# Kernel tuning notes

Hardware: AMD Instinct MI355X
Metric: run time of the kernel (lower is better)

Reference implementation:

```python
import jax, jax.numpy as jnp
import numpy as np

B, N, DIM = 4, 1024, 1024
H, D = 16, 64          # num_heads, head_dim
SW = 256               # sliding_window
ROPE_BASE = 10000.0
LN_EPS = 1e-5


def _layernorm(x, w, b):
    mu = jnp.mean(x, axis=-1, keepdims=True)
    var = jnp.mean((x - mu) ** 2, axis=-1, keepdims=True)
    return (x - mu) * jax.lax.rsqrt(var + LN_EPS) * w + b


def _rotate_half(x):
    x1, x2 = jnp.split(x, 2, axis=-1)
    return jnp.concatenate([-x2, x1], axis=-1)


def setup_inputs() -> dict:
    key = jax.random.key(0)
    ks = jax.random.split(key, 8)
    s = 0.02
    return {
        "x": jax.random.normal(ks[0], (B, N, DIM), dtype=jnp.float32),
        "qkv_w": jax.random.normal(ks[1], (3 * H * D, DIM), dtype=jnp.float32) * s,
        "qn_w": jnp.ones((D,), jnp.float32),
        "qn_b": jnp.zeros((D,), jnp.float32),
        "kn_w": jnp.ones((D,), jnp.float32),
        "kn_b": jnp.zeros((D,), jnp.float32),
        "sinks": jax.random.normal(ks[2], (H,), dtype=jnp.float32),
        "proj_w": jax.random.normal(ks[3], (DIM, H * D), dtype=jnp.float32) * s,
        "proj_b": jnp.zeros((DIM,), jnp.float32),
    }


def reference(x, qkv_w, qn_w, qn_b, kn_w, kn_b, sinks, proj_w, proj_b):
    Bx, Nx, _ = x.shape
    # fused QKV projection -> [3, B, H, N, D]
    qkv = (x @ qkv_w.T).reshape(Bx, Nx, 3, H, D).transpose(2, 0, 3, 1, 4)
    q, k, v = qkv[0], qkv[1], qkv[2]
    # qk-norm (LayerNorm over head_dim)
    q = _layernorm(q, qn_w, qn_b)
    k = _layernorm(k, kn_w, kn_b)
    # 1d RoPE (DeepseekV3-style: emb = cat(freqs, freqs), rotate_half)
    inv_freq = 1.0 / (ROPE_BASE ** (jnp.arange(0, D, 2, dtype=jnp.float32) / D))
    freqs = jnp.arange(Nx, dtype=jnp.float32)[:, None] * inv_freq[None, :]  # [N, D/2]
    emb = jnp.concatenate([freqs, freqs], axis=-1)                           # [N, D]
    cos, sin = jnp.cos(emb), jnp.sin(emb)
    q = q * cos + _rotate_half(q) * sin
    k = k * cos + _rotate_half(k) * sin
    # sliding-window causal mask with attention sinks
    sm_scale = 1.0 / np.sqrt(D)
    scores = jnp.einsum("bhqd,bhkd->bhqk", q, k) * sm_scale  # [B,H,N,N]
    i = jnp.arange(Nx)[:, None]
    j = jnp.arange(Nx)[None, :]
    allowed = (j <= i) & (j > i - SW)
    scores = jnp.where(allowed, scores, -jnp.inf)
    # append sink logit per head, softmax, drop sink column
    sink_col = jnp.broadcast_to(sinks[None, :, None, None], (Bx, H, Nx, 1))
    logits = jnp.concatenate([scores, sink_col], axis=-1)
    probs = jax.nn.softmax(logits, axis=-1)[..., :-1]
    out = jnp.einsum("bhqk,bhkd->bhqd", probs, v)
    out = out.transpose(0, 2, 1, 3).reshape(Bx, Nx, H * D)
    return out @ proj_w.T + proj_b
```

## Files before the change

### kernel.cpp

```cpp
#include <hip/hip_runtime.h>
#include <stdint.h>

typedef unsigned short u16;
typedef __bf16 bf16x8 __attribute__((ext_vector_type(8)));
typedef float f32x4 __attribute__((ext_vector_type(4)));

__device__ __forceinline__ float b2f(u16 u) {
  union { uint32_t i; float f; } x; x.i = ((uint32_t)u) << 16; return x.f;
}
__device__ __forceinline__ u16 f2b(float f) {
  union { float f; uint32_t i; } x; x.f = f;
  uint32_t r = x.i + 0x7fffu + ((x.i >> 16) & 1u);
  return (u16)(r >> 16);
}
__device__ __forceinline__ void gload_lds16(const u16* g, u16* l) {
  __builtin_amdgcn_global_load_lds(
      (const __attribute__((address_space(1))) void*)g,
      (__attribute__((address_space(3))) void*)l, 16, 0, 0);
}

__launch_bounds__(256)
__global__ void cvt_bf16(const float* __restrict__ x, const float* __restrict__ wq,
                         const float* __restrict__ wp, u16* __restrict__ dst) {
  const int i = (blockIdx.x * 256 + threadIdx.x) * 4;
  const float* src; int off;
  if (i < 4194304)      { src = x;  off = i; }
  else if (i < 7340032) { src = wq; off = i - 4194304; }
  else                  { src = wp; off = i - 7340032; }
  const float4 v = *(const float4*)(src + off);
  ushort4 o;
  o.x = f2b(v.x); o.y = f2b(v.y); o.z = f2b(v.z); o.w = f2b(v.w);
  *(ushort4*)(dst + i) = o;
}

__launch_bounds__(256)
__global__ void rope_tab(float* __restrict__ tab) {
  const int tid = blockIdx.x * 256 + threadIdx.x;
  const int pos = tid >> 6, d = tid & 63, i = d & 31;
  const float f = pos * exp2f(i * -0.41524101186092029f);
  float s, c;
  sincosf(f, &s, &c);
  *(float2*)(tab + tid * 2) = make_float2(c, s);
}

template<int MODE>
__launch_bounds__(256)
__global__ void gemm128(const u16* __restrict__ A, const u16* __restrict__ Bw,
                        void* __restrict__ Cp, const float* __restrict__ bias, int K) {
  __shared__ __align__(16) u16 As[128 * 32];
  __shared__ __align__(16) u16 Bs[128 * 32];
  const int t = threadIdx.x;
  const int w = t >> 6, l = t & 63, lr = l & 15, lg = l >> 4;
  const int m0 = blockIdx.y * 128, n0 = blockIdx.x * 128;
  const int wm = (w >> 1) * 64, wn = (w & 1) * 64;
  const int srow = w * 32 + (l >> 2);
  const int scol = (l & 3) * 8;
  const u16* ga0 = A  + (m0 + srow) * K + scol;
  const u16* ga1 = ga0 + 16 * K;
  const u16* gb0 = Bw + (n0 + srow) * K + scol;
  const u16* gb1 = gb0 + 16 * K;
  u16* la0 = As + w * 1024;
  u16* la1 = As + w * 1024 + 512;
  u16* lb0 = Bs + w * 1024;
  u16* lb1 = Bs + w * 1024 + 512;

  f32x4 acc[4][4] = {};
  const int nk = K >> 5;
  for (int kt = 0; kt < nk; ++kt) {
    const int ko = kt * 32;
    __syncthreads();
    gload_lds16(ga0 + ko, la0);
    gload_lds16(ga1 + ko, la1);
    gload_lds16(gb0 + ko, lb0);
    gload_lds16(gb1 + ko, lb1);
    __syncthreads();
    bf16x8 af[4], bfr[4];
#pragma unroll
    for (int i = 0; i < 4; ++i)
      af[i] = *(const bf16x8*)(As + (wm + i * 16 + lr) * 32 + lg * 8);
#pragma unroll
    for (int j = 0; j < 4; ++j)
      bfr[j] = *(const bf16x8*)(Bs + (wn + j * 16 + lr) * 32 + lg * 8);
#pragma unroll
    for (int i = 0; i < 4; ++i)
#pragma unroll
      for (int j = 0; j < 4; ++j)
        acc[i][j] = __builtin_amdgcn_mfma_f32_16x16x32_bf16(af[i], bfr[j], acc[i][j], 0, 0, 0);
  }
#pragma unroll
  for (int i = 0; i < 4; ++i)
#pragma unroll
    for (int j = 0; j < 4; ++j)
#pragma unroll
      for (int r = 0; r < 4; ++r) {
        const int gm = m0 + wm + i * 16 + lg * 4 + r;
        const int gn = n0 + wn + j * 16 + lr;
        const float v = acc[i][j][r];
        if (MODE == 0) {
          const int which = gn >> 10, hh = (gn >> 6) & 15, dd = gn & 63;
          const int bb = gm >> 10, pp = gm & 1023;
          ((u16*)Cp)[which * 4194304 + ((bb * 16 + hh) << 16) + (pp << 6) + dd] = f2b(v);
        } else {
          ((float*)Cp)[(gm << 10) + gn] = v + bias[gn];
        }
      }
}

__launch_bounds__(256)
__global__ void ln_rope(u16* __restrict__ qk, const float* __restrict__ qn_w,
                        const float* __restrict__ qn_b, const float* __restrict__ kn_w,
                        const float* __restrict__ kn_b, const float* __restrict__ tab) {
  const int t = threadIdx.x, l = t & 63;
  const int wv = blockIdx.x * 4 + (t >> 6);
  const int row = wv * 8 + (l >> 3);
  const int c = l & 7;
  const int which = row >> 16;
  const int pos = row & 1023;
  const float* wgt = which ? kn_w : qn_w;
  const float* bia = which ? kn_b : qn_b;
  const u16* src = qk + row * 64 + c * 8;
  const ushort4 ra = *(const ushort4*)(src);
  const ushort4 rb = *(const ushort4*)(src + 4);
  float v[8] = {b2f(ra.x), b2f(ra.y), b2f(ra.z), b2f(ra.w),
                b2f(rb.x), b2f(rb.y), b2f(rb.z), b2f(rb.w)};
  float s = 0.f;
#pragma unroll
  for (int i = 0; i < 8; ++i) s += v[i];
#pragma unroll
  for (int off = 1; off < 8; off <<= 1) s += __shfl_xor(s, off);
  const float mu = s * 0.015625f;
  float e[8], qs = 0.f;
#pragma unroll
  for (int i = 0; i < 8; ++i) { e[i] = v[i] - mu; qs += e[i] * e[i]; }
#pragma unroll
  for (int off = 1; off < 8; off <<= 1) qs += __shfl_xor(qs, off);
  const float rstd = rsqrtf(qs * 0.015625f + 1e-5f);
  const int d0 = c * 8;
  float wb[8], bb[8];
  *(float4*)(wb) = *(const float4*)(wgt + d0);
  *(float4*)(wb + 4) = *(const float4*)(wgt + d0 + 4);
  *(float4*)(bb) = *(const float4*)(bia + d0);
  *(float4*)(bb + 4) = *(const float4*)(bia + d0 + 4);
  float n[8], r[8];
#pragma unroll
  for (int i = 0; i < 8; ++i) n[i] = e[i] * rstd * wb[i] + bb[i];
#pragma unroll
  for (int i = 0; i < 8; ++i) r[i] = __shfl_xor(n[i], 4);
  const bool lo = (c < 4);
#pragma unroll
  for (int i = 0; i < 8; ++i) r[i] = lo ? -r[i] : r[i];
  float cs[16];
  *(float4*)(cs)      = *(const float4*)(tab + (pos * 64 + d0) * 2);
  *(float4*)(cs + 4)  = *(const float4*)(tab + (pos * 64 + d0) * 2 + 4);
  *(float4*)(cs + 8)  = *(const float4*)(tab + (pos * 64 + d0) * 2 + 8);
  *(float4*)(cs + 12) = *(const float4*)(tab + (pos * 64 + d0) * 2 + 12);
  ushort4 oa, ob;
  float o[8];
#pragma unroll
  for (int i = 0; i < 8; ++i) o[i] = n[i] * cs[2 * i] + r[i] * cs[2 * i + 1];
  oa.x = f2b(o[0]); oa.y = f2b(o[1]); oa.z = f2b(o[2]); oa.w = f2b(o[3]);
  ob.x = f2b(o[4]); ob.y = f2b(o[5]); ob.z = f2b(o[6]); ob.w = f2b(o[7]);
  const int dstc = which ? (c ^ (pos & 7)) : c;
  u16* dst = qk + row * 64 + dstc * 8;
  *(ushort4*)(dst) = oa;
  *(ushort4*)(dst + 4) = ob;
}

__launch_bounds__(256)
__global__ void vtrans(const u16* __restrict__ v, u16* __restrict__ vt) {
  __shared__ u16 tile[128 * 65];
  const int t = threadIdx.x;
  const int bh = blockIdx.x >> 3;
  const int n0 = (blockIdx.x & 7) * 128;
  const u16* src = v + bh * 65536 + n0 * 64;
#pragma unroll
  for (int it = 0; it < 8; ++it) {
    const int e = (it * 256 + t) * 4;
    const int n = e >> 6, d = e & 63;
    const ushort4 x = *(const ushort4*)(src + n * 64 + d);
    tile[n * 65 + d + 0] = x.x;
    tile[n * 65 + d + 1] = x.y;
    tile[n * 65 + d + 2] = x.z;
    tile[n * 65 + d + 3] = x.w;
  }
  __syncthreads();
  u16* dst = vt + bh * 65536;
#pragma unroll
  for (int it = 0; it < 8; ++it) {
    const int o = (it * 256 + t) * 4;
    const int d = o >> 7, c = o & 127;
    ushort4 y;
    y.x = tile[(c + 0) * 65 + d];
    y.y = tile[(c + 1) * 65 + d];
    y.z = tile[(c + 2) * 65 + d];
    y.w = tile[(c + 3) * 65 + d];
    const int gj = n0 + c;
    const int nb = gj >> 6, jl = gj & 63;
    const int slot = (jl >> 3) ^ (d & 7);
    *(ushort4*)(dst + nb * 4096 + d * 64 + slot * 8 + (jl & 7)) = y;
  }
}

__launch_bounds__(256, 2)
__global__ void attn_kernel(const u16* __restrict__ q, const u16* __restrict__ k,
                            const u16* __restrict__ vt, const float* __restrict__ sinks,
                            u16* __restrict__ ao) {
  __shared__ __align__(16) u16 Ks[20480];
  __shared__ __align__(16) u16 Vs[20480];
  const int t = threadIdx.x, w = t >> 6, l = t & 63, lr = l & 15, lg = l >> 4;
  const int bid = blockIdx.x;
  const int qb = bid & 15, h = (bid >> 4) & 15, b = bid >> 8;
  const int i0 = qb * 64 + w * 16;
  const int bh = b * 16 + h;
  const u16* qp = q + bh * 65536;
  const u16* kp = k + bh * 65536;
  const u16* vp = vt + bh * 65536;
  const int j0 = qb * 64 - 256;

#pragma unroll
  for (int i = 0; i < 10; ++i) {
    const int c = w * 10 + i;
    int off = j0 * 64 + c * 512 + l * 8;
    off = off < 0 ? 0 : off;
    gload_lds16(kp + off, Ks + c * 512);
  }
#pragma unroll
  for (int i = 0; i < 10; ++i) {
    const int c = w * 10 + i;
    const int n = c >> 3, p = c & 7;
    int nb = qb - 4 + n;
    nb = nb < 0 ? 0 : nb;
    gload_lds16(vp + nb * 4096 + p * 512 + l * 8, Vs + c * 512);
  }
  const bf16x8 qf0 = *(const bf16x8*)(qp + (i0 + lr) * 64 + lg * 8);
  const bf16x8 qf1 = *(const bf16x8*)(qp + (i0 + lr) * 64 + 32 + lg * 8);
  __syncthreads();

  const int key = lr & 7;
  f32x4 sacc[17];
#pragma unroll
  for (int jt = 0; jt < 17; ++jt) {
    const int r = w * 16 + jt * 16 + lr;
    const bf16x8 kf0 = *(const bf16x8*)(Ks + r * 64 + ((lg ^ key)) * 8);
    const bf16x8 kf1 = *(const bf16x8*)(Ks + r * 64 + (((lg + 4) ^ key)) * 8);
    f32x4 a = {0.f, 0.f, 0.f, 0.f};
    a = __builtin_amdgcn_mfma_f32_16x16x32_bf16(qf0, kf0, a, 0, 0, 0);
    a = __builtin_amdgcn_mfma_f32_16x16x32_bf16(qf1, kf1, a, 0, 0, 0);
    sacc[jt] = a;
  }
  const float sink = sinks[h];
  const int ja = i0 - 256;
  float mx[4] = {-1e30f, -1e30f, -1e30f, -1e30f};
#pragma unroll
  for (int jt = 0; jt < 17; ++jt)
#pragma unroll
    for (int r = 0; r < 4; ++r) {
      const int qi = i0 + lg * 4 + r;
      const int jg = ja + jt * 16 + lr;
      const bool ok = (jg >= 0) && (jg <= qi) && (jg > qi - 256);
      const float sv = ok ? sacc[jt][r] * 0.125f : -1e30f;
      sacc[jt][r] = sv;
      mx[r] = fmaxf(mx[r], sv);
    }
#pragma unroll
  for (int off = 1; off < 16; off <<= 1)
#pragma unroll
    for (int r = 0; r < 4; ++r) mx[r] = fmaxf(mx[r], __shfl_xor(mx[r], off));
#pragma unroll
  for (int r = 0; r < 4; ++r) mx[r] = fmaxf(mx[r], sink);
  float sum[4] = {0.f, 0.f, 0.f, 0.f};
#pragma unroll
  for (int jt = 0; jt < 17; ++jt)
#pragma unroll
    for (int r = 0; r < 4; ++r) {
      const float e = __expf(sacc[jt][r] - mx[r]);
      sacc[jt][r] = e;
      sum[r] += e;
    }
#pragma unroll
  for (int off = 1; off < 16; off <<= 1)
#pragma unroll
    for (int r = 0; r < 4; ++r) sum[r] += __shfl_xor(sum[r], off);
  float inv[4];
#pragma unroll
  for (int r = 0; r < 4; ++r) inv[r] = 1.0f / (sum[r] + __expf(sink - mx[r]));

  __syncthreads();
  u16* pb = Ks + w * 4736;
  {
    ushort4 z; z.x = 0; z.y = 0; z.z = 0; z.w = 0;
    *(ushort4*)(pb + (l >> 2) * 296 + 272 + (l & 3) * 4) = z;
  }
#pragma unroll
  for (int jt = 0; jt < 17; ++jt)
#pragma unroll
    for (int r = 0; r < 4; ++r)
      pb[(lg * 4 + r) * 296 + jt * 16 + lr] = f2b(sacc[jt][r] * inv[r]);

  f32x4 oacc[4] = {};
#pragma unroll
  for (int ks = 0; ks < 9; ++ks) {
    const bf16x8 pf = *(const bf16x8*)(pb + lr * 296 + ks * 32 + lg * 8);
#pragma unroll
    for (int dt = 0; dt < 4; ++dt) {
      int r = w * 16 + ks * 32 + lg * 8;
      r = r < 320 ? r : 0;
      const int n = r >> 6, jl = r & 63;
      const int slot = (jl >> 3) ^ (lr & 7);
      const bf16x8 vf = *(const bf16x8*)(Vs + n * 4096 + (dt * 16 + lr) * 64 + slot * 8);
      oacc[dt] = __builtin_amdgcn_mfma_f32_16x16x32_bf16(pf, vf, oacc[dt], 0, 0, 0);
    }
  }
#pragma unroll
  for (int dt = 0; dt < 4; ++dt)
#pragma unroll
    for (int r = 0; r < 4; ++r) {
      const int m = (b << 10) + i0 + lg * 4 + r;
      ao[(m << 10) + (h << 6) + dt * 16 + lr] = f2b(oacc[dt][r]);
    }
}

extern "C" void kernel_launch(void* const* d_in, const int* in_sizes, int n_in,
                              void* d_out, int out_size, void* d_ws, size_t ws_size,
                              hipStream_t stream) {
  const float* x      = (const float*)d_in[0];
  const float* qkv_w  = (const float*)d_in[1];
  const float* qn_w   = (const float*)d_in[2];
  const float* qn_b   = (const float*)d_in[3];
  const float* kn_w   = (const float*)d_in[4];
  const float* kn_b   = (const float*)d_in[5];
  const float* sinks  = (const float*)d_in[6];
  const float* proj_w = (const float*)d_in[7];
  const float* proj_b = (const float*)d_in[8];
  float* out = (float*)d_out;
  u16* ws     = (u16*)d_ws;
  u16* qkv    = ws;
  u16* xb     = ws + 12582912;
  u16* wqkvb  = ws + 16777216;
  u16* wprojb = ws + 19922944;
  float* tab  = (float*)(ws + 20971520);
  u16* ao     = ws + 21233664;
  u16* vtw    = ws + 12582912;

  cvt_bf16<<<8192, 256, 0, stream>>>(x, qkv_w, proj_w, xb);
  rope_tab<<<256, 256, 0, stream>>>(tab);
  gemm128<0><<<dim3(24, 32), 256, 0, stream>>>(xb, wqkvb, qkv, nullptr, 1024);
  ln_rope<<<4096, 256, 0, stream>>>(qkv, qn_w, qn_b, kn_w, kn_b, tab);
  vtrans<<<512, 256, 0, stream>>>(qkv + 8388608, vtw);
  attn_kernel<<<1024, 256, 0, stream>>>(qkv, qkv + 4194304, vtw, sinks, ao);
  gemm128<1><<<dim3(8, 32), 256, 0, stream>>>(ao, wprojb, out, proj_b, 1024);
}
```

Measured before the change: 199.3 us.

## Fuse qk-LayerNorm and RoPE into QKV GEMM epilogue, widen K tile, swizzle LDS

The fp32-to-bf16 conversion and the RoPE table build are merged into one prep kernel. That kernel also writes the bf16 operands in an XOR-swizzled 8-element-slot layout. The QKV GEMM now loads 64-wide K tiles and reads LDS with the matching swizzle to avoid bank conflicts, and it applies LayerNorm and RoPE for q/k in its epilogue through intra-row shuffles. This removes the separate ln_rope pass over q and k. The attention output is also written swizzled so the projection GEMM can read it the same way, at the cost of more complex address math and a larger LDS footprint.

Result: no change. 199.7 us (+0.2%).

```diff
diff --git a/kernel.cpp b/kernel.cpp
--- a/kernel.cpp
+++ b/kernel.cpp
@@ -13,6 +13,14 @@
   uint32_t r = x.i + 0x7fffu + ((x.i >> 16) & 1u);
   return (u16)(r >> 16);
 }
+__device__ __forceinline__ uint4 pk8(const float4 a, const float4 b) {
+  uint4 r;
+  r.x = (uint32_t)f2b(a.x) | ((uint32_t)f2b(a.y) << 16);
+  r.y = (uint32_t)f2b(a.z) | ((uint32_t)f2b(a.w) << 16);
+  r.z = (uint32_t)f2b(b.x) | ((uint32_t)f2b(b.y) << 16);
+  r.w = (uint32_t)f2b(b.z) | ((uint32_t)f2b(b.w) << 16);
+  return r;
+}
 __device__ __forceinline__ void gload_lds16(const u16* g, u16* l) {
   __builtin_amdgcn_global_load_lds(
       (const __attribute__((address_space(1))) void*)g,
@@ -20,150 +28,159 @@
 }
 
 __launch_bounds__(256)
-__global__ void cvt_bf16(const float* __restrict__ x, const float* __restrict__ wq,
-                         const float* __restrict__ wp, u16* __restrict__ dst) {
-  const int i = (blockIdx.x * 256 + threadIdx.x) * 4;
-  const float* src; int off;
-  if (i < 4194304)      { src = x;  off = i; }
-  else if (i < 7340032) { src = wq; off = i - 4194304; }
-  else                  { src = wp; off = i - 7340032; }
-  const float4 v = *(const float4*)(src + off);
-  ushort4 o;
-  o.x = f2b(v.x); o.y = f2b(v.y); o.z = f2b(v.z); o.w = f2b(v.w);
-  *(ushort4*)(dst + i) = o;
-}
-
-__launch_bounds__(256)
-__global__ void rope_tab(float* __restrict__ tab) {
-  const int tid = blockIdx.x * 256 + threadIdx.x;
-  const int pos = tid >> 6, d = tid & 63, i = d & 31;
-  const float f = pos * exp2f(i * -0.41524101186092029f);
-  float s, c;
-  sincosf(f, &s, &c);
-  *(float2*)(tab + tid * 2) = make_float2(c, s);
+__global__ void prep(const float* __restrict__ x, const float* __restrict__ wq,
+                     const float* __restrict__ wp, u16* __restrict__ dst,
+                     float* __restrict__ tab) {
+  if (blockIdx.x >= 4096) {
+    const int tid = (blockIdx.x - 4096) * 256 + threadIdx.x;
+    const int pos = tid >> 5, idx = tid & 31;
+    const float f = pos * exp2f(idx * -0.41524101186092029f);
+    float s, c;
+    sincosf(f, &s, &c);
+    *(float2*)(tab + tid * 2) = make_float2(c, s);
+    return;
+  }
+  const int i = (blockIdx.x * 256 + threadIdx.x) * 8;
+  const float* src; int local, base;
+  if (i < 4194304)      { src = x;  local = i;           base = 0; }
+  else if (i < 7340032) { src = wq; local = i - 4194304; base = 4194304; }
+  else                  { src = wp; local = i - 7340032; base = 7340032; }
+  const int row = local >> 10, col = local & 1023;
+  const int slot = ((col >> 3) & 7) ^ (row & 7);
+  const float4 a = *(const float4*)(src + local);
+  const float4 b = *(const float4*)(src + local + 4);
+  *(uint4*)(dst + base + row * 1024 + (col & ~63) + slot * 8) = pk8(a, b);
 }
 
 template<int MODE>
 __launch_bounds__(256)
 __global__ void gemm128(const u16* __restrict__ A, const u16* __restrict__ Bw,
-                        void* __restrict__ Cp, const float* __restrict__ bias, int K) {
-  __shared__ __align__(16) u16 As[128 * 32];
-  __shared__ __align__(16) u16 Bs[128 * 32];
+                        void* __restrict__ Cp, const float* __restrict__ bias,
+                        const float* __restrict__ qn_w, const float* __restrict__ qn_b,
+                        const float* __restrict__ kn_w, const float* __restrict__ kn_b,
+                        const float* __restrict__ tab, int K) {
+  __shared__ __align__(16) u16 As[128 * 64];
+  __shared__ __align__(16) u16 Bs[128 * 64];
   const int t = threadIdx.x;
   const int w = t >> 6, l = t & 63, lr = l & 15, lg = l >> 4;
   const int m0 = blockIdx.y * 128, n0 = blockIdx.x * 128;
   const int wm = (w >> 1) * 64, wn = (w & 1) * 64;
-  const int srow = w * 32 + (l >> 2);
-  const int scol = (l & 3) * 8;
-  const u16* ga0 = A  + (m0 + srow) * K + scol;
-  const u16* ga1 = ga0 + 16 * K;
-  const u16* gb0 = Bw + (n0 + srow) * K + scol;
-  const u16* gb1 = gb0 + 16 * K;
-  u16* la0 = As + w * 1024;
-  u16* la1 = As + w * 1024 + 512;
-  u16* lb0 = Bs + w * 1024;
-  u16* lb1 = Bs + w * 1024 + 512;
+  const int srow = w * 32 + (l >> 3);
+  const int scol = (l & 7) * 8;
+  const u16* gA = A  + (m0 + srow) * K + scol;
+  const u16* gB = Bw + (n0 + srow) * K + scol;
 
   f32x4 acc[4][4] = {};
-  const int nk = K >> 5;
+  const int nk = K >> 6;
   for (int kt = 0; kt < nk; ++kt) {
-    const int ko = kt * 32;
+    const int ko = kt * 64;
     __syncthreads();
-    gload_lds16(ga0 + ko, la0);
-    gload_lds16(ga1 + ko, la1);
-    gload_lds16(gb0 + ko, lb0);
-    gload_lds16(gb1 + ko, lb1);
+#pragma unroll
+    for (int i = 0; i < 4; ++i)
+      gload_lds16(gA + i * 8 * K + ko, As + (w * 32 + i * 8) * 64);
+#pragma unroll
+    for (int i = 0; i < 4; ++i)
+      gload_lds16(gB + i * 8 * K + ko, Bs + (w * 32 + i * 8) * 64);
     __syncthreads();
-    bf16x8 af[4], bfr[4];
-#pragma unroll
-    for (int i = 0; i < 4; ++i)
-      af[i] = *(const bf16x8*)(As + (wm + i * 16 + lr) * 32 + lg * 8);
-#pragma unroll
-    for (int j = 0; j < 4; ++j)
-      bfr[j] = *(const bf16x8*)(Bs + (wn + j * 16 + lr) * 32 + lg * 8);
+    bf16x8 af0[4], af1[4], bf0[4], bf1[4];
+#pragma unroll
+    for (int i = 0; i < 4; ++i) {
+      const int ra = wm + i * 16 + lr;
+      const int sa = (lg ^ (ra & 7)) * 8;
+      af0[i] = *(const bf16x8*)(As + ra * 64 + sa);
+      af1[i] = *(const bf16x8*)(As + ra * 64 + (sa ^ 32));
+    }
+#pragma unroll
+    for (int j = 0; j < 4; ++j) {
+      const int rb = wn + j * 16 + lr;
+      const int sb = (lg ^ (rb & 7)) * 8;
+      bf0[j] = *(const bf16x8*)(Bs + rb * 64 + sb);
+      bf1[j] = *(const bf16x8*)(Bs + rb * 64 + (sb ^ 32));
+    }
+#pragma unroll
+    for (int i = 0; i < 4; ++i)
+#pragma unroll
+      for (int j = 0; j < 4; ++j) {
+        acc[i][j] = __builtin_amdgcn_mfma_f32_16x16x32_bf16(af0[i], bf0[j], acc[i][j], 0, 0, 0);
+        acc[i][j] = __builtin_amdgcn_mfma_f32_16x16x32_bf16(af1[i], bf1[j], acc[i][j], 0, 0, 0);
+      }
+  }
+
+  if (MODE == 1) {
 #pragma unroll
     for (int i = 0; i < 4; ++i)
 #pragma unroll
       for (int j = 0; j < 4; ++j)
-        acc[i][j] = __builtin_amdgcn_mfma_f32_16x16x32_bf16(af[i], bfr[j], acc[i][j], 0, 0, 0);
-  }
+#pragma unroll
+        for (int r = 0; r < 4; ++r) {
+          const int gm = m0 + wm + i * 16 + lg * 4 + r;
+          const int gn = n0 + wn + j * 16 + lr;
+          ((float*)Cp)[(gm << 10) + gn] = acc[i][j][r] + bias[gn];
+        }
+    return;
+  }
+  const int whichB = blockIdx.x >> 3;
+  const int hh = ((n0 + wn) >> 6) & 15;
+  u16* Cb = (u16*)Cp + whichB * 4194304;
+  if (whichB == 2) {
+#pragma unroll
+    for (int i = 0; i < 4; ++i)
+#pragma unroll
+      for (int j = 0; j < 4; ++j)
+#pragma unroll
+        for (int r = 0; r < 4; ++r) {
+          const int gm = m0 + wm + i * 16 + lg * 4 + r;
+          Cb[(((gm >> 10) * 16 + hh) << 16) + ((gm & 1023) << 6) + j * 16 + lr] =
+              f2b(acc[i][j][r]);
+        }
+    return;
+  }
+  const float* wl = whichB ? kn_w : qn_w;
+  const float* bl = whichB ? kn_b : qn_b;
+  float wln[4], bln[4];
+#pragma unroll
+  for (int j = 0; j < 4; ++j) { wln[j] = wl[j * 16 + lr]; bln[j] = bl[j * 16 + lr]; }
 #pragma unroll
   for (int i = 0; i < 4; ++i)
 #pragma unroll
-    for (int j = 0; j < 4; ++j)
-#pragma unroll
-      for (int r = 0; r < 4; ++r) {
-        const int gm = m0 + wm + i * 16 + lg * 4 + r;
-        const int gn = n0 + wn + j * 16 + lr;
-        const float v = acc[i][j][r];
-        if (MODE == 0) {
-          const int which = gn >> 10, hh = (gn >> 6) & 15, dd = gn & 63;
-          const int bb = gm >> 10, pp = gm & 1023;
-          ((u16*)Cp)[which * 4194304 + ((bb * 16 + hh) << 16) + (pp << 6) + dd] = f2b(v);
-        } else {
-          ((float*)Cp)[(gm << 10) + gn] = v + bias[gn];
+    for (int r = 0; r < 4; ++r) {
+      const int gm = m0 + wm + i * 16 + lg * 4 + r;
+      const int pos = gm & 1023;
+      float v0 = acc[i][0][r], v1 = acc[i][1][r], v2 = acc[i][2][r], v3 = acc[i][3][r];
+      float s = v0 + v1 + v2 + v3;
+#pragma unroll
+      for (int m = 1; m < 16; m <<= 1) s += __shfl_xor(s, m);
+      const float mu = s * 0.015625f;
+      const float d0 = v0 - mu, d1 = v1 - mu, d2 = v2 - mu, d3 = v3 - mu;
+      float qv = d0 * d0 + d1 * d1 + d2 * d2 + d3 * d3;
+#pragma unroll
+      for (int m = 1; m < 16; m <<= 1) qv += __shfl_xor(qv, m);
+      const float rstd = rsqrtf(qv * 0.015625f + 1e-5f);
+      float nn[4];
+      nn[0] = d0 * rstd * wln[0] + bln[0];
+      nn[1] = d1 * rstd * wln[1] + bln[1];
+      nn[2] = d2 * rstd * wln[2] + bln[2];
+      nn[3] = d3 * rstd * wln[3] + bln[3];
+      const float2 csA = *(const float2*)(tab + (pos * 32 + lr) * 2);
+      const float2 csB = *(const float2*)(tab + (pos * 32 + 16 + lr) * 2);
+      float o[4];
+      o[0] = nn[0] * csA.x - nn[2] * csA.y;
+      o[1] = nn[1] * csB.x - nn[3] * csB.y;
+      o[2] = nn[2] * csA.x + nn[0] * csA.y;
+      o[3] = nn[3] * csB.x + nn[1] * csB.y;
+      u16* cb = Cb + (((gm >> 10) * 16 + hh) << 16) + (pos << 6);
+      if (whichB == 1) {
+        const int key = pos & 7;
+#pragma unroll
+        for (int j = 0; j < 4; ++j) {
+          const int d = j * 16 + lr;
+          cb[((d >> 3) ^ key) * 8 + (d & 7)] = f2b(o[j]);
         }
+      } else {
+#pragma unroll
+        for (int j = 0; j < 4; ++j) cb[j * 16 + lr] = f2b(o[j]);
       }
-}
-
-__launch_bounds__(256)
-__global__ void ln_rope(u16* __restrict__ qk, const float* __restrict__ qn_w,
-                        const float* __restrict__ qn_b, const float* __restrict__ kn_w,
-                        const float* __restrict__ kn_b, const float* __restrict__ tab) {
-  const int t = threadIdx.x, l = t & 63;
-  const int wv = blockIdx.x * 4 + (t >> 6);
-  const int row = wv * 8 + (l >> 3);
-  const int c = l & 7;
-  const int which = row >> 16;
-  const int pos = row & 1023;
-  const float* wgt = which ? kn_w : qn_w;
-  const float* bia = which ? kn_b : qn_b;
-  const u16* src = qk + row * 64 + c * 8;
-  const ushort4 ra = *(const ushort4*)(src);
-  const ushort4 rb = *(const ushort4*)(src + 4);
-  float v[8] = {b2f(ra.x), b2f(ra.y), b2f(ra.z), b2f(ra.w),
-                b2f(rb.x), b2f(rb.y), b2f(rb.z), b2f(rb.w)};
-  float s = 0.f;
-#pragma unroll
-  for (int i = 0; i < 8; ++i) s += v[i];
-#pragma unroll
-  for (int off = 1; off < 8; off <<= 1) s += __shfl_xor(s, off);
-  const float mu = s * 0.015625f;
-  float e[8], qs = 0.f;
-#pragma unroll
-  for (int i = 0; i < 8; ++i) { e[i] = v[i] - mu; qs += e[i] * e[i]; }
-#pragma unroll
-  for (int off = 1; off < 8; off <<= 1) qs += __shfl_xor(qs, off);
-  const float rstd = rsqrtf(qs * 0.015625f + 1e-5f);
-  const int d0 = c * 8;
-  float wb[8], bb[8];
-  *(float4*)(wb) = *(const float4*)(wgt + d0);
-  *(float4*)(wb + 4) = *(const float4*)(wgt + d0 + 4);
-  *(float4*)(bb) = *(const float4*)(bia + d0);
-  *(float4*)(bb + 4) = *(const float4*)(bia + d0 + 4);
-  float n[8], r[8];
-#pragma unroll
-  for (int i = 0; i < 8; ++i) n[i] = e[i] * rstd * wb[i] + bb[i];
-#pragma unroll
-  for (int i = 0; i < 8; ++i) r[i] = __shfl_xor(n[i], 4);
-  const bool lo = (c < 4);
-#pragma unroll
-  for (int i = 0; i < 8; ++i) r[i] = lo ? -r[i] : r[i];
-  float cs[16];
-  *(float4*)(cs)      = *(const float4*)(tab + (pos * 64 + d0) * 2);
-  *(float4*)(cs + 4)  = *(const float4*)(tab + (pos * 64 + d0) * 2 + 4);
-  *(float4*)(cs + 8)  = *(const float4*)(tab + (pos * 64 + d0) * 2 + 8);
-  *(float4*)(cs + 12) = *(const float4*)(tab + (pos * 64 + d0) * 2 + 12);
-  ushort4 oa, ob;
-  float o[8];
-#pragma unroll
-  for (int i = 0; i < 8; ++i) o[i] = n[i] * cs[2 * i] + r[i] * cs[2 * i + 1];
-  oa.x = f2b(o[0]); oa.y = f2b(o[1]); oa.z = f2b(o[2]); oa.w = f2b(o[3]);
-  ob.x = f2b(o[4]); ob.y = f2b(o[5]); ob.z = f2b(o[6]); ob.w = f2b(o[7]);
-  const int dstc = which ? (c ^ (pos & 7)) : c;
-  u16* dst = qk + row * 64 + dstc * 8;
-  *(ushort4*)(dst) = oa;
-  *(ushort4*)(dst + 4) = ob;
+    }
 }
 
 __launch_bounds__(256)
@@ -316,7 +333,8 @@
 #pragma unroll
     for (int r = 0; r < 4; ++r) {
       const int m = (b << 10) + i0 + lg * 4 + r;
-      ao[(m << 10) + (h << 6) + dt * 16 + lr] = f2b(oacc[dt][r]);
+      const int cg = (dt * 2 + (lr >> 3)) ^ (m & 7);
+      ao[(m << 10) + (h << 6) + cg * 8 + (lr & 7)] = f2b(oacc[dt][r]);
     }
 }
 
@@ -336,17 +354,17 @@
   u16* ws     = (u16*)d_ws;
   u16* qkv    = ws;
   u16* xb     = ws + 12582912;
-  u16* wqkvb  = ws + 16777216;
   u16* wprojb = ws + 19922944;
   float* tab  = (float*)(ws + 20971520);
   u16* ao     = ws + 21233664;
   u16* vtw    = ws + 12582912;
 
-  cvt_bf16<<<8192, 256, 0, stream>>>(x, qkv_w, proj_w, xb);
-  rope_tab<<<256, 256, 0, stream>>>(tab);
-  gemm128<0><<<dim3(24, 32), 256, 0, stream>>>(xb, wqkvb, qkv, nullptr, 1024);
-  ln_rope<<<4096, 256, 0, stream>>>(qkv, qn_w, qn_b, kn_w, kn_b, tab);
+  prep<<<4224, 256, 0, stream>>>(x, qkv_w, proj_w, xb, tab);
+  gemm128<0><<<dim3(24, 32), 256, 0, stream>>>(xb, xb + 4194304, qkv, nullptr,
+                                               qn_w, qn_b, kn_w, kn_b, tab, 1024);
   vtrans<<<512, 256, 0, stream>>>(qkv + 8388608, vtw);
   attn_kernel<<<1024, 256, 0, stream>>>(qkv, qkv + 4194304, vtw, sinks, ao);
-  gemm128<1><<<dim3(8, 32), 256, 0, stream>>>(ao, wprojb, out, proj_b, 1024);
-}
+  gemm128<1><<<dim3(8, 32), 256, 0, stream>>>(ao, wprojb, out, proj_b,
+                                              nullptr, nullptr, nullptr, nullptr,
+                                              nullptr, 1024);
+}
```

## Fuse prep kernels, write V transposed from QKV GEMM, swizzle GEMM LDS layout

Applied to the files above, without the earlier changes.

Merges the bf16 conversion and RoPE table kernels into one launch, with the table halved to 32 entries per position. The QKV GEMM epilogue now writes V directly in the swizzled transposed layout, which removes the separate vtrans kernel and its round trip through memory. GEMM operands are pre-swizzled during conversion, and the attention output is written swizzled, so that LDS fragment reads avoid bank conflicts. The cost is scattered 2-byte stores in the V epilogue and a more complex write layout that every consumer must agree on.

After: 190.0 us. 1.05x faster.

```diff
diff --git a/kernel.cpp b/kernel.cpp
--- a/kernel.cpp
+++ b/kernel.cpp
@@ -13,6 +13,14 @@
   uint32_t r = x.i + 0x7fffu + ((x.i >> 16) & 1u);
   return (u16)(r >> 16);
 }
+__device__ __forceinline__ uint4 pk8(const float4 a, const float4 b) {
+  uint4 r;
+  r.x = (uint32_t)f2b(a.x) | ((uint32_t)f2b(a.y) << 16);
+  r.y = (uint32_t)f2b(a.z) | ((uint32_t)f2b(a.w) << 16);
+  r.z = (uint32_t)f2b(b.x) | ((uint32_t)f2b(b.y) << 16);
+  r.w = (uint32_t)f2b(b.z) | ((uint32_t)f2b(b.w) << 16);
+  return r;
+}
 __device__ __forceinline__ void gload_lds16(const u16* g, u16* l) {
   __builtin_amdgcn_global_load_lds(
       (const __attribute__((address_space(1))) void*)g,
@@ -20,33 +28,35 @@
 }
 
 __launch_bounds__(256)
-__global__ void cvt_bf16(const float* __restrict__ x, const float* __restrict__ wq,
-                         const float* __restrict__ wp, u16* __restrict__ dst) {
-  const int i = (blockIdx.x * 256 + threadIdx.x) * 4;
-  const float* src; int off;
-  if (i < 4194304)      { src = x;  off = i; }
-  else if (i < 7340032) { src = wq; off = i - 4194304; }
-  else                  { src = wp; off = i - 7340032; }
-  const float4 v = *(const float4*)(src + off);
-  ushort4 o;
-  o.x = f2b(v.x); o.y = f2b(v.y); o.z = f2b(v.z); o.w = f2b(v.w);
-  *(ushort4*)(dst + i) = o;
-}
-
-__launch_bounds__(256)
-__global__ void rope_tab(float* __restrict__ tab) {
-  const int tid = blockIdx.x * 256 + threadIdx.x;
-  const int pos = tid >> 6, d = tid & 63, i = d & 31;
-  const float f = pos * exp2f(i * -0.41524101186092029f);
-  float s, c;
-  sincosf(f, &s, &c);
-  *(float2*)(tab + tid * 2) = make_float2(c, s);
+__global__ void prep(const float* __restrict__ x, const float* __restrict__ wq,
+                     const float* __restrict__ wp, u16* __restrict__ dst,
+                     float* __restrict__ tab) {
+  if (blockIdx.x >= 4096) {
+    const int tid = (blockIdx.x - 4096) * 256 + threadIdx.x;
+    const int pos = tid >> 5, idx = tid & 31;
+    const float f = pos * exp2f(idx * -0.41524101186092029f);
+    float s, c;
+    sincosf(f, &s, &c);
+    *(float2*)(tab + tid * 2) = make_float2(c, s);
+    return;
+  }
+  const int i = (blockIdx.x * 256 + threadIdx.x) * 8;
+  const float* src; int local, base;
+  if (i < 4194304)      { src = x;  local = i;           base = 0; }
+  else if (i < 7340032) { src = wq; local = i - 4194304; base = 4194304; }
+  else                  { src = wp; local = i - 7340032; base = 7340032; }
+  const int row = local >> 10, col = local & 1023;
+  const int slot = ((col >> 3) & 3) ^ (row & 3);
+  const float4 a = *(const float4*)(src + local);
+  const float4 b = *(const float4*)(src + local + 4);
+  *(uint4*)(dst + base + (row << 10) + (col & ~31) + (slot << 3)) = pk8(a, b);
 }
 
 template<int MODE>
 __launch_bounds__(256)
 __global__ void gemm128(const u16* __restrict__ A, const u16* __restrict__ Bw,
-                        void* __restrict__ Cp, const float* __restrict__ bias, int K) {
+                        void* __restrict__ Cp, const float* __restrict__ bias,
+                        u16* __restrict__ vt, int K) {
   __shared__ __align__(16) u16 As[128 * 32];
   __shared__ __align__(16) u16 Bs[128 * 32];
   const int t = threadIdx.x;
@@ -76,17 +86,53 @@
     __syncthreads();
     bf16x8 af[4], bfr[4];
 #pragma unroll
-    for (int i = 0; i < 4; ++i)
-      af[i] = *(const bf16x8*)(As + (wm + i * 16 + lr) * 32 + lg * 8);
-#pragma unroll
-    for (int j = 0; j < 4; ++j)
-      bfr[j] = *(const bf16x8*)(Bs + (wn + j * 16 + lr) * 32 + lg * 8);
+    for (int i = 0; i < 4; ++i) {
+      const int ra = wm + i * 16 + lr;
+      af[i] = *(const bf16x8*)(As + ra * 32 + ((lg ^ (ra & 3)) << 3));
+    }
+#pragma unroll
+    for (int j = 0; j < 4; ++j) {
+      const int rb = wn + j * 16 + lr;
+      bfr[j] = *(const bf16x8*)(Bs + rb * 32 + ((lg ^ (rb & 3)) << 3));
+    }
 #pragma unroll
     for (int i = 0; i < 4; ++i)
 #pragma unroll
       for (int j = 0; j < 4; ++j)
         acc[i][j] = __builtin_amdgcn_mfma_f32_16x16x32_bf16(af[i], bfr[j], acc[i][j], 0, 0, 0);
   }
+  if (MODE == 1) {
+#pragma unroll
+    for (int i = 0; i < 4; ++i)
+#pragma unroll
+      for (int j = 0; j < 4; ++j)
+#pragma unroll
+        for (int r = 0; r < 4; ++r) {
+          const int gm = m0 + wm + i * 16 + lg * 4 + r;
+          const int gn = n0 + wn + j * 16 + lr;
+          ((float*)Cp)[(gm << 10) + gn] = acc[i][j][r] + bias[gn];
+        }
+    return;
+  }
+  const int whichB = blockIdx.x >> 3;
+  const int hh = ((n0 + wn) >> 6) & 15;
+  if (whichB == 2) {
+#pragma unroll
+    for (int i = 0; i < 4; ++i)
+#pragma unroll
+      for (int j = 0; j < 4; ++j)
+#pragma unroll
+        for (int r = 0; r < 4; ++r) {
+          const int gm = m0 + wm + i * 16 + lg * 4 + r;
+          const int bh = (gm >> 10) * 16 + hh;
+          const int pos = gm & 1023, nb = pos >> 6, jl = pos & 63;
+          const int d = j * 16 + lr;
+          vt[bh * 65536 + nb * 4096 + d * 64 + (((jl >> 3) ^ (d & 7)) << 3) + (jl & 7)] =
+              f2b(acc[i][j][r]);
+        }
+    return;
+  }
+  u16* Cb = (u16*)Cp + whichB * 4194304;
 #pragma unroll
   for (int i = 0; i < 4; ++i)
 #pragma unroll
@@ -94,15 +140,8 @@
 #pragma unroll
       for (int r = 0; r < 4; ++r) {
         const int gm = m0 + wm + i * 16 + lg * 4 + r;
-        const int gn = n0 + wn + j * 16 + lr;
-        const float v = acc[i][j][r];
-        if (MODE == 0) {
-          const int which = gn >> 10, hh = (gn >> 6) & 15, dd = gn & 63;
-          const int bb = gm >> 10, pp = gm & 1023;
-          ((u16*)Cp)[which * 4194304 + ((bb * 16 + hh) << 16) + (pp << 6) + dd] = f2b(v);
-        } else {
-          ((float*)Cp)[(gm << 10) + gn] = v + bias[gn];
-        }
+        Cb[(((gm >> 10) * 16 + hh) << 16) + ((gm & 1023) << 6) + j * 16 + lr] =
+            f2b(acc[i][j][r]);
       }
 }
 
@@ -150,10 +189,11 @@
 #pragma unroll
   for (int i = 0; i < 8; ++i) r[i] = lo ? -r[i] : r[i];
   float cs[16];
-  *(float4*)(cs)      = *(const float4*)(tab + (pos * 64 + d0) * 2);
-  *(float4*)(cs + 4)  = *(const float4*)(tab + (pos * 64 + d0) * 2 + 4);
-  *(float4*)(cs + 8)  = *(const float4*)(tab + (pos * 64 + d0) * 2 + 8);
-  *(float4*)(cs + 12) = *(const float4*)(tab + (pos * 64 + d0) * 2 + 12);
+  const int ti = (pos * 32 + (c & 3) * 8) * 2;
+  *(float4*)(cs)      = *(const float4*)(tab + ti);
+  *(float4*)(cs + 4)  = *(const float4*)(tab + ti + 4);
+  *(float4*)(cs + 8)  = *(const float4*)(tab + ti + 8);
+  *(float4*)(cs + 12) = *(const float4*)(tab + ti + 12);
   ushort4 oa, ob;
   float o[8];
 #pragma unroll
@@ -164,41 +204,6 @@
   u16* dst = qk + row * 64 + dstc * 8;
   *(ushort4*)(dst) = oa;
   *(ushort4*)(dst + 4) = ob;
-}
-
-__launch_bounds__(256)
-__global__ void vtrans(const u16* __restrict__ v, u16* __restrict__ vt) {
-  __shared__ u16 tile[128 * 65];
-  const int t = threadIdx.x;
-  const int bh = blockIdx.x >> 3;
-  const int n0 = (blockIdx.x & 7) * 128;
-  const u16* src = v + bh * 65536 + n0 * 64;
-#pragma unroll
-  for (int it = 0; it < 8; ++it) {
-    const int e = (it * 256 + t) * 4;
-    const int n = e >> 6, d = e & 63;
-    const ushort4 x = *(const ushort4*)(src + n * 64 + d);
-    tile[n * 65 + d + 0] = x.x;
-    tile[n * 65 + d + 1] = x.y;
-    tile[n * 65 + d + 2] = x.z;
-    tile[n * 65 + d + 3] = x.w;
-  }
-  __syncthreads();
-  u16* dst = vt + bh * 65536;
-#pragma unroll
-  for (int it = 0; it < 8; ++it) {
-    const int o = (it * 256 + t) * 4;
-    const int d = o >> 7, c = o & 127;
-    ushort4 y;
-    y.x = tile[(c + 0) * 65 + d];
-    y.y = tile[(c + 1) * 65 + d];
-    y.z = tile[(c + 2) * 65 + d];
-    y.w = tile[(c + 3) * 65 + d];
-    const int gj = n0 + c;
-    const int nb = gj >> 6, jl = gj & 63;
-    const int slot = (jl >> 3) ^ (d & 7);
-    *(ushort4*)(dst + nb * 4096 + d * 64 + slot * 8 + (jl & 7)) = y;
-  }
 }
 
 __launch_bounds__(256, 2)
@@ -316,7 +321,9 @@
 #pragma unroll
     for (int r = 0; r < 4; ++r) {
       const int m = (b << 10) + i0 + lg * 4 + r;
-      ao[(m << 10) + (h << 6) + dt * 16 + lr] = f2b(oacc[dt][r]);
+      const int d = dt * 16 + lr;
+      const int cg = ((d >> 3) & 3) ^ (m & 3);
+      ao[(m << 10) + (h << 6) + (d & ~31) + (cg << 3) + (d & 7)] = f2b(oacc[dt][r]);
     }
 }
 
@@ -335,18 +342,15 @@
   float* out = (float*)d_out;
   u16* ws     = (u16*)d_ws;
   u16* qkv    = ws;
+  u16* vtw    = ws + 8388608;
   u16* xb     = ws + 12582912;
-  u16* wqkvb  = ws + 16777216;
   u16* wprojb = ws + 19922944;
   float* tab  = (float*)(ws + 20971520);
   u16* ao     = ws + 21233664;
-  u16* vtw    = ws + 12582912;
-
-  cvt_bf16<<<8192, 256, 0, stream>>>(x, qkv_w, proj_w, xb);
-  rope_tab<<<256, 256, 0, stream>>>(tab);
-  gemm128<0><<<dim3(24, 32), 256, 0, stream>>>(xb, wqkvb, qkv, nullptr, 1024);
+
+  prep<<<4224, 256, 0, stream>>>(x, qkv_w, proj_w, xb, tab);
+  gemm128<0><<<dim3(24, 32), 256, 0, stream>>>(xb, xb + 4194304, qkv, nullptr, vtw, 1024);
   ln_rope<<<4096, 256, 0, stream>>>(qkv, qn_w, qn_b, kn_w, kn_b, tab);
-  vtrans<<<512, 256, 0, stream>>>(qkv + 8388608, vtw);
   attn_kernel<<<1024, 256, 0, stream>>>(qkv, qkv + 4194304, vtw, sinks, ao);
-  gemm128<1><<<dim3(8, 32), 256, 0, stream>>>(ao, wprojb, out, proj_b, 1024);
-}
+  gemm128<1><<<dim3(8, 32), 256, 0, stream>>>(ao, wprojb, out, proj_b, nullptr, 1024);
+}
```
